# Kernel tuning notes

Measured on AMD Instinct MI355X. Metric: run time of the kernel, lower is better.

Reference implementation:

```python
import jax, jax.numpy as jnp
import numpy as np

N = 250_000          # total event nodes across the batch
E = 1_000_000        # directed edges (radius-graph style, avg degree 4)
B = 25               # graphs in the batch
BS = N // B          # nodes per graph (contiguous blocks)
NX, NY = 8, 9        # ceil(120/16), ceil(100/12) voxel cells for MaxPooling
NC = NX * NY         # 72 voxel cells per graph
M = B * NC           # pooled node slots (empty cells kept but masked)
GRIDS = 16           # MaxPoolingX: 4x4 cells of size (30,25) over 120x100
NOUT = 2
EPS = 1e-5


def spline_basis(p):
    # SplineConv basis: kernel_size=2 per dim, degree=1 open B-spline, dim=3.
    # basis_s(p) = prod_d (p_d if bit_d(s) else 1 - p_d), s = b0 + 2*b1 + 4*b2
    p = jnp.clip(p, 0.0, 1.0)
    cols = []
    for s in range(8):
        w = jnp.ones(p.shape[0], p.dtype)
        for d in range(3):
            w = w * (p[:, d] if (s >> d) & 1 else 1.0 - p[:, d])
        cols.append(w)
    return jnp.stack(cols, axis=1)  # [E, 8]


def spline_conv(x, src, dst, basis, W, emask, num_nodes):
    # SplineConv with aggr='mean', bias=False, root_weight=False
    xj = x[src]                                   # [E, Cin] gather
    msg = jnp.zeros((xj.shape[0], W.shape[2]), x.dtype)
    for s in range(W.shape[0]):                   # 8 kernel weight matrices
        msg = msg + basis[:, s:s + 1] * (xj @ W[s])
    msg = msg * emask[:, None]
    out = jax.ops.segment_sum(msg, dst, num_segments=num_nodes)
    deg = jax.ops.segment_sum(emask, dst, num_segments=num_nodes)
    return out / jnp.maximum(deg, 1.0)[:, None]


def batch_norm(x, gamma, beta, mask=None):
    # BatchNorm1d over nodes (training-mode batch statistics, biased var)
    if mask is None:
        mean = x.mean(axis=0)
        var = jnp.mean((x - mean) ** 2, axis=0)
        return (x - mean) * jax.lax.rsqrt(var + EPS) * gamma + beta
    m = mask.astype(x.dtype)[:, None]
    cnt = jnp.maximum(m.sum(), 1.0)
    mean = (x * m).sum(axis=0) / cnt
    var = (((x - mean) ** 2) * m).sum(axis=0) / cnt
    return ((x - mean) * jax.lax.rsqrt(var + EPS) * gamma + beta) * m


def _forward(x, pos, edge_attr, ws, gs, bs, fc_w, edge_index, batch):
    src, dst = edge_index[0], edge_index[1]
    basis = spline_basis(edge_attr)
    em = jnp.ones((src.shape[0],), x.dtype)
    for i in range(5):  # conv1..conv5 + norm + relu on the full event graph
        x = spline_conv(x, src, dst, basis, ws[i], em, N)
        x = jax.nn.relu(batch_norm(x, gs[i], bs[i]))
    # ---- MaxPooling: voxel grid (16,12) over pos[:, :2], coarsen graph ----
    cx = jnp.clip(jnp.floor(pos[:, 0] / 16.0).astype(jnp.int32), 0, NX - 1)
    cy = jnp.clip(jnp.floor(pos[:, 1] / 12.0).astype(jnp.int32), 0, NY - 1)
    cluster = batch * NC + cy * NX + cx           # [N] -> [0, M)
    cnt = jax.ops.segment_sum(jnp.ones((N,), x.dtype), cluster, num_segments=M)
    nmask = cnt > 0                               # non-empty voxel cells
    xp = jax.ops.segment_max(x, cluster, num_segments=M)
    xp = jnp.where(nmask[:, None], xp, 0.0)       # [M, 32]
    pp = jax.ops.segment_sum(pos, cluster, num_segments=M) / jnp.maximum(cnt, 1.0)[:, None]
    # coarsen edges: remap via cluster, drop self loops, coalesce duplicates
    key = cluster[src] * M + cluster[dst]
    key = jnp.where(cluster[src] == cluster[dst], M * M, key)
    ks = jnp.sort(key)
    dup = jnp.concatenate([jnp.zeros((1,), bool), ks[1:] == ks[:-1]])
    evalid = (ks < M * M) & (~dup)
    rs = jnp.where(evalid, ks // M, 0)
    cs = jnp.where(evalid, ks % M, 0)
    emf = evalid.astype(x.dtype)
    # Cartesian(norm=True, cat=False) on pooled positions
    d = (pp[cs] - pp[rs]) * emf[:, None]
    maxv = jnp.maximum(jnp.max(jnp.abs(d)), 1e-9)
    ea2 = d / (2.0 * maxv) + 0.5
    basis2 = spline_basis(ea2)
    for i in range(5, 7):  # conv6, conv7 on pooled graph
        xp = spline_conv(xp, rs, cs, basis2, ws[i], emf, M)
        xp = jax.nn.relu(batch_norm(xp, gs[i], bs[i], nmask))
    # ---- MaxPoolingX: (30,25) voxel grid -> 4x4 = 16 cells per graph ----
    bcl = jnp.arange(M, dtype=jnp.int32) // NC    # batch id of each cluster
    gx = jnp.clip(jnp.floor(pp[:, 0] / 30.0).astype(jnp.int32), 0, 3)
    gy = jnp.clip(jnp.floor(pp[:, 1] / 25.0).astype(jnp.int32), 0, 3)
    seg = jnp.where(nmask, bcl * GRIDS + gy * 4 + gx, B * GRIDS)
    xg = jax.ops.segment_max(xp, seg, num_segments=B * GRIDS + 1)[:B * GRIDS]
    xg = jnp.where(jnp.isfinite(xg), xg, 0.0)     # empty cells -> 0
    feat = xg.reshape(B, GRIDS * 32)              # [B, 512]
    return feat @ fc_w.T                          # [B, NOUT]


def setup_inputs() -> dict:
    key = jax.random.key(0)
    k = jax.random.split(key, 16)
    x = jax.random.uniform(k[0], (N, 1), dtype=jnp.float32)
    pos = jax.random.uniform(k[1], (N, 3), dtype=jnp.float32) * jnp.array([120.0, 100.0, 1.0], jnp.float32)
    batch = (jnp.arange(N) // BS).astype(jnp.int32)
    src = jax.random.randint(k[2], (E,), 0, N, dtype=jnp.int32)
    dst = (src // BS) * BS + jax.random.randint(k[3], (E,), 0, BS, dtype=jnp.int32)
    edge_index = jnp.stack([src, dst])
    edge_attr = jax.random.uniform(k[4], (E, 3), dtype=jnp.float32)
    chans = [1, 8, 16, 16, 16, 32, 32, 32]
    inp = {"x": x, "pos": pos, "edge_attr": edge_attr}
    for i in range(7):
        cin, cout = chans[i], chans[i + 1]
        inp[f"w{i+1}"] = jax.random.normal(k[5 + i], (8, cin, cout), jnp.float32) / np.sqrt(8.0 * cin)
    for i in range(7):
        inp[f"g{i+1}"] = jnp.ones((chans[i + 1],), jnp.float32)
    for i in range(7):
        inp[f"b{i+1}"] = jnp.zeros((chans[i + 1],), jnp.float32)
    inp["fc_w"] = jax.random.normal(k[12], (NOUT, GRIDS * 32), jnp.float32) * 0.05
    inp["edge_index"] = edge_index
    inp["batch"] = batch
    return inp


def reference(x, pos, edge_attr, w1, w2, w3, w4, w5, w6, w7,
              g1, g2, g3, g4, g5, g6, g7,
              b1, b2, b3, b4, b5, b6, b7, fc_w, edge_index, batch):
    ws = (w1, w2, w3, w4, w5, w6, w7)
    gs = (g1, g2, g3, g4, g5, g6, g7)
    bs = (b1, b2, b3, b4, b5, b6, b7)
    return _forward(x, pos, edge_attr, ws, gs, bs, fc_w, edge_index, batch)
```

## Files before the change

kernel.cpp:

```cpp
#include <hip/hip_runtime.h>

constexpr int NN   = 250000;
constexpr int NE   = 1000000;
constexpr int NBm  = 25;
constexpr int BSg  = NN / NBm;
constexpr int NCc  = 72;
constexpr int MM   = NBm * NCc;
constexpr int PRES = NBm * NCc * NCc;
constexpr int NBK  = NBm * 16;
constexpr float EPSbn = 1e-5f;


__global__ __launch_bounds__(256) void k_deg(const int* __restrict__ dst, int* __restrict__ deg, int n) {
    int e = blockIdx.x * 256 + threadIdx.x;
    if (e < n) atomicAdd(&deg[dst[e]], 1);
}

__global__ __launch_bounds__(256) void k_dhist(const int* __restrict__ deg, const int* __restrict__ batch,
                                               int* __restrict__ dhist, int n) {
    __shared__ int h[NBK];
    int tid = threadIdx.x;
    for (int i = tid; i < NBK; i += 256) h[i] = 0;
    __syncthreads();
    int i = blockIdx.x * 256 + tid;
    if (i < n) atomicAdd(&h[batch[i] * 16 + (15 - min(deg[i], 15))], 1);
    __syncthreads();
    for (int b = tid; b < NBK; b += 256) if (h[b]) atomicAdd(&dhist[b], h[b]);
}

__global__ __launch_bounds__(256) void k_dscan(const int* __restrict__ dhist, int* __restrict__ dcur) {
    __shared__ int tmp[NBK];
    int t = threadIdx.x;
    for (int i = t; i < NBK; i += 256) tmp[i] = dhist[i];
    __syncthreads();
    if (t == 0) { int run = 0; for (int i = 0; i < NBK; i++) { int v = tmp[i]; tmp[i] = run; run += v; } }
    __syncthreads();
    for (int i = t; i < NBK; i += 256) dcur[i] = tmp[i];
}

__global__ __launch_bounds__(256) void k_dscat(const int* __restrict__ deg, const int* __restrict__ batch,
                                               const float* __restrict__ x_in,
                                               int* __restrict__ dcur, int* __restrict__ pinv,
                                               int* __restrict__ deg_p, float* __restrict__ xin_p, int n) {
    __shared__ int lcnt[NBK];
    __shared__ int gbase[NBK];
    int tid = threadIdx.x;
    for (int i = tid; i < NBK; i += 256) lcnt[i] = 0;
    __syncthreads();
    int i = blockIdx.x * 256 + tid;
    int b = 0, rank = 0;
    if (i < n) {
        b = batch[i] * 16 + (15 - min(deg[i], 15));
        rank = atomicAdd(&lcnt[b], 1);
    }
    __syncthreads();
    for (int k = tid; k < NBK; k += 256)
        if (lcnt[k]) gbase[k] = atomicAdd(&dcur[k], lcnt[k]);
    __syncthreads();
    if (i < n) {
        int slot = gbase[b] + rank;
        pinv[i] = slot;
        deg_p[slot] = deg[i];
        xin_p[slot] = x_in[i];
    }
}

__global__ __launch_bounds__(256) void k_scan1(const int* __restrict__ in, int n,
                                               int* __restrict__ outEx, int* __restrict__ bsum) {
    __shared__ int lds[256];
    int t = threadIdx.x;
    int base = blockIdx.x * 2048;
    int v[8]; int s = 0;
#pragma unroll
    for (int i = 0; i < 8; i++) { int idx = base + t * 8 + i; v[i] = (idx < n) ? in[idx] : 0; s += v[i]; }
    lds[t] = s; __syncthreads();
    for (int o = 1; o < 256; o <<= 1) {
        int x = (t >= o) ? lds[t - o] : 0; __syncthreads();
        lds[t] += x; __syncthreads();
    }
    if (t == 255) bsum[blockIdx.x] = lds[255];
    int run = lds[t] - s;
#pragma unroll
    for (int i = 0; i < 8; i++) { int idx = base + t * 8 + i; if (idx < n) outEx[idx] = run; run += v[i]; }
}

__global__ __launch_bounds__(256) void k_scan2(int* bsum, int nb) {
    __shared__ int l[256];
    int t = threadIdx.x;
    int v = (t < nb) ? bsum[t] : 0;
    l[t] = v; __syncthreads();
    for (int o = 1; o < 256; o <<= 1) {
        int x = (t >= o) ? l[t - o] : 0; __syncthreads();
        l[t] += x; __syncthreads();
    }
    if (t < nb) bsum[t] = l[t] - v;
}

__global__ __launch_bounds__(256) void k_scan3(int* __restrict__ outEx, int n, const int* __restrict__ bsum) {
    int i = blockIdx.x * 256 + threadIdx.x;
    if (i < n) outEx[i] += bsum[i >> 11];
}

__global__ __launch_bounds__(256) void k_scatter(const int* __restrict__ src, const int* __restrict__ dst,
                                                 const float* __restrict__ ea, const int* __restrict__ offx,
                                                 const int* __restrict__ pinv,
                                                 int* __restrict__ cursor, float4* __restrict__ erec, int n) {
    int e = blockIdx.x * 256 + threadIdx.x;
    if (e >= n) return;
    int d = pinv[dst[e]];
    int j = offx[d] + atomicAdd(&cursor[d], 1);
    float p0 = fminf(fmaxf(ea[e * 3 + 0], 0.f), 1.f);
    float p1 = fminf(fmaxf(ea[e * 3 + 1], 0.f), 1.f);
    float p2 = fminf(fmaxf(ea[e * 3 + 2], 0.f), 1.f);
    erec[j] = make_float4(__int_as_float(pinv[src[e]]), p0, p1, p2);
}

__global__ __launch_bounds__(256) void k_cluster(const float* __restrict__ pos, const int* __restrict__ pinv,
                                                 int* __restrict__ cluster, int* __restrict__ cluster_p,
                                                 int* __restrict__ cnt, float* __restrict__ ppsum) {
    __shared__ int lcnt[NCc];
    __shared__ float lpp[NCc * 3];
    int tid = threadIdx.x;
    int g = blockIdx.x >> 3, part = blockIdx.x & 7;
    for (int i = tid; i < NCc; i += 256) lcnt[i] = 0;
    for (int i = tid; i < NCc * 3; i += 256) lpp[i] = 0.f;
    __syncthreads();
    int base = g * BSg + part * (BSg / 8);
    int lim = BSg / 8;
    for (int k = tid; k < lim; k += 256) {
        int i = base + k;
        float px = pos[i * 3], py = pos[i * 3 + 1], pz = pos[i * 3 + 2];
        int cx = min(max((int)floorf(px / 16.f), 0), 7);
        int cy = min(max((int)floorf(py / 12.f), 0), 8);
        int lc = cy * 8 + cx;
        cluster[i] = g * NCc + lc;
        cluster_p[pinv[i]] = g * NCc + lc;
        atomicAdd(&lcnt[lc], 1);
        atomicAdd(&lpp[lc * 3 + 0], px);
        atomicAdd(&lpp[lc * 3 + 1], py);
        atomicAdd(&lpp[lc * 3 + 2], pz);
    }
    __syncthreads();
    for (int c = tid; c < NCc; c += 256) {
        if (lcnt[c]) {
            atomicAdd(&cnt[g * NCc + c], lcnt[c]);
            atomicAdd(&ppsum[(g * NCc + c) * 3 + 0], lpp[c * 3 + 0]);
            atomicAdd(&ppsum[(g * NCc + c) * 3 + 1], lpp[c * 3 + 1]);
            atomicAdd(&ppsum[(g * NCc + c) * 3 + 2], lpp[c * 3 + 2]);
        }
    }
}

__global__ __launch_bounds__(256) void k_coarse(const int* __restrict__ src, const int* __restrict__ dst,
                                                const int* __restrict__ cluster, unsigned char* __restrict__ presence,
                                                int n) {
    int e = blockIdx.x * 256 + threadIdx.x;
    if (e >= n) return;
    int r = cluster[src[e]], c = cluster[dst[e]];
    if (r == c) return;
    int g = r / NCc;
    presence[g * (NCc * NCc) + (r % NCc) * NCc + (c % NCc)] = 1;
}

__global__ __launch_bounds__(256) void k_fpp(const int* __restrict__ cnt, const float* __restrict__ ppsum,
                                             float* __restrict__ pp, int* __restrict__ nmask, int* __restrict__ nmc) {
    int m = blockIdx.x * 256 + threadIdx.x;
    if (m >= MM) return;
    int c = cnt[m];
    float inv = 1.f / (float)max(c, 1);
    pp[m * 3 + 0] = ppsum[m * 3 + 0] * inv;
    pp[m * 3 + 1] = ppsum[m * 3 + 1] * inv;
    pp[m * 3 + 2] = ppsum[m * 3 + 2] * inv;
    nmask[m] = (c > 0);
    if (c > 0) atomicAdd(nmc, 1);
}

__global__ __launch_bounds__(256) void k_maxv(const unsigned char* __restrict__ presence, const float* __restrict__ pp,
                                              float* __restrict__ maxv) {
    int i = blockIdx.x * 256 + threadIdx.x;
    float m = 0.f;
    if (i < PRES && presence[i]) {
        int g = i / (NCc * NCc), rem = i % (NCc * NCc);
        int r = g * NCc + rem / NCc, c = g * NCc + rem % NCc;
        float d0 = fabsf(pp[c * 3 + 0] - pp[r * 3 + 0]);
        float d1 = fabsf(pp[c * 3 + 1] - pp[r * 3 + 1]);
        float d2 = fabsf(pp[c * 3 + 2] - pp[r * 3 + 2]);
        m = fmaxf(fmaxf(d0, d1), d2);
    }
    for (int o = 32; o; o >>= 1) m = fmaxf(m, __shfl_xor(m, o));
    if ((threadIdx.x & 63) == 0) atomicMax((int*)maxv, __float_as_int(m));
}


template <int CIN, int COUT, int TPN, bool BN>
__global__ __launch_bounds__(256) void k_conv(
    const float* __restrict__ x, const float4* __restrict__ erec,
    const int* __restrict__ off, const int* __restrict__ deg,
    const float* __restrict__ W, const float* __restrict__ st,
    const float* __restrict__ gam, const float* __restrict__ bet, float invcnt,
    float* __restrict__ out, float* __restrict__ stG, int nwaves) {
    constexpr int CPT = CIN / TPN;
    constexpr int SLICE = COUT + 4;
    constexpr int NPW = 128 / TPN;
    constexpr int CPG = (BSg + NPW - 1) / NPW;
    constexpr int WPG = (CPG + 1) / 2;
    constexpr int NH = (COUT > 16) ? 2 : 1;
    constexpr int OH = COUT / NH;
    constexpr int CWH = OH / TPN;
    __shared__ float Ws[8 * CIN * SLICE];
    __shared__ float ssum[COUT], ssq[COUT];
    int tid = threadIdx.x;
    for (int idx = tid; idx < 8 * CIN * COUT; idx += 256) {
        int s = idx / (CIN * COUT), r = idx % (CIN * COUT);
        int ci = r / COUT, co = r % COUT;
        int t_ = ci / CPT, i_ = ci % CPT;
        Ws[((s * CPT + i_) * TPN + t_) * SLICE + co] = W[idx];
    }
    if (tid < COUT) { ssum[tid] = 0.f; ssq[tid] = 0.f; }
    __syncthreads();

    int w = blockIdx.x * 4 + (tid >> 6);
    int lane = tid & 63;
    int t = lane & (TPN - 1);
    int qi = lane / TPN;
    bool wact = (w < nwaves);
    int g = wact ? (w / WPG) : 0;
    int p = wact ? (w % WPG) : 0;

    float sc[CPT], sh[CPT];
    if constexpr (BN) {
#pragma unroll
        for (int i = 0; i < CPT; i++) {
            int c = t * CPT + i;
            float mean = st[c] * invcnt;
            float var = st[CIN + c] * invcnt - mean * mean;
            float s = rsqrtf(var + EPSbn) * gam[c];
            sc[i] = s; sh[i] = bet[c] - mean * s;
        }
    }

    for (int rep = 0; rep < 2; rep++) {
        if (!wact) break;
        int c = rep ? (CPG - 1 - p) : p;
        if (rep && c == p) break;
        int base = g * BSg + c * NPW;
        int lim = min(NPW, BSg - c * NPW);
        int no = 2 * qi;
        bool act = no < lim;
        int n0 = base + no;

        float agg[2][8 * CPT];
#pragma unroll
        for (int r = 0; r < 2; r++)
#pragma unroll
            for (int i = 0; i < 8 * CPT; i++) agg[r][i] = 0.f;

        int dg0 = 0, dg1 = 0, jb0 = 0, jb1 = 0;
        if (act) {
            jb0 = off[n0];     dg0 = deg[n0];
            jb1 = off[n0 + 1]; dg1 = deg[n0 + 1];
        }
        int mx = max(dg0, dg1);
        int cl0 = max(dg0 - 1, 0), cl1 = max(dg1 - 1, 0);
        float4 rec0 = erec[min(jb0, NE - 1)];
        float4 rec1 = erec[min(jb1, NE - 1)];
        for (int m = 0; m < mx; m++) {
            int s0 = __float_as_int(rec0.x);
            int s1 = __float_as_int(rec1.x);
            const float* xs0 = &x[(size_t)s0 * CIN + t * CPT];
            const float* xs1 = &x[(size_t)s1 * CIN + t * CPT];
            float xv0[CPT], xv1[CPT];
            if constexpr (CPT == 4) {
                float4 v0 = *(const float4*)xs0;
                float4 v1 = *(const float4*)xs1;
                xv0[0] = v0.x; xv0[1] = v0.y; xv0[2] = v0.z; xv0[3] = v0.w;
                xv1[0] = v1.x; xv1[1] = v1.y; xv1[2] = v1.z; xv1[3] = v1.w;
            } else if constexpr (CPT == 8) {
#pragma unroll
                for (int i = 0; i < 8; i += 4) {
                    float4 v0 = *(const float4*)&xs0[i];
                    float4 v1 = *(const float4*)&xs1[i];
                    xv0[i] = v0.x; xv0[i + 1] = v0.y; xv0[i + 2] = v0.z; xv0[i + 3] = v0.w;
                    xv1[i] = v1.x; xv1[i + 1] = v1.y; xv1[i + 2] = v1.z; xv1[i + 3] = v1.w;
                }
            } else {
#pragma unroll
                for (int i = 0; i < CPT; i++) { xv0[i] = xs0[i]; xv1[i] = xs1[i]; }
            }
            float4 nrec0 = erec[jb0 + min(m + 1, cl0)];
            float4 nrec1 = erec[jb1 + min(m + 1, cl1)];
            float f0 = (m < dg0) ? 1.f : 0.f;
            float f1 = (m < dg1) ? 1.f : 0.f;
            if constexpr (BN) {
#pragma unroll
                for (int i = 0; i < CPT; i++) {
                    float a = xv0[i] * sc[i] + sh[i]; xv0[i] = a > 0.f ? a : 0.f;
                    float b = xv1[i] * sc[i] + sh[i]; xv1[i] = b > 0.f ? b : 0.f;
                }
            }
            {
                float p0 = rec0.y, p1 = rec0.z;
                float p2 = rec0.w * f0, q2 = (1.f - rec0.w) * f0;
                float q0 = 1.f - p0, q1 = 1.f - p1;
                float a00 = q0 * q1, a10 = p0 * q1, a01 = q0 * p1, a11 = p0 * p1;
                float bbv[8] = {a00 * q2, a10 * q2, a01 * q2, a11 * q2,
                                a00 * p2, a10 * p2, a01 * p2, a11 * p2};
#pragma unroll
                for (int k = 0; k < 8; k++)
#pragma unroll
                    for (int i = 0; i < CPT; i++) agg[0][k * CPT + i] += bbv[k] * xv0[i];
            }
            {
                float p0 = rec1.y, p1 = rec1.z;
                float p2 = rec1.w * f1, q2 = (1.f - rec1.w) * f1;
                float q0 = 1.f - p0, q1 = 1.f - p1;
                float a00 = q0 * q1, a10 = p0 * q1, a01 = q0 * p1, a11 = p0 * p1;
                float bbv[8] = {a00 * q2, a10 * q2, a01 * q2, a11 * q2,
                                a00 * p2, a10 * p2, a01 * p2, a11 * p2};
#pragma unroll
                for (int k = 0; k < 8; k++)
#pragma unroll
                    for (int i = 0; i < CPT; i++) agg[1][k * CPT + i] += bbv[k] * xv1[i];
            }
            rec0 = nrec0; rec1 = nrec1;
        }

        float inv0 = 1.f / (float)max(dg0, 1);
        float inv1 = 1.f / (float)max(dg1, 1);

#pragma unroll
        for (int h = 0; h < NH; h++) {
            float o0[OH], o1[OH];
#pragma unroll
            for (int c2 = 0; c2 < OH; c2++) { o0[c2] = 0.f; o1[c2] = 0.f; }
#pragma unroll
            for (int k = 0; k < 8; k++)
#pragma unroll
                for (int i = 0; i < CPT; i++) {
                    float a0 = agg[0][k * CPT + i];
                    float a1 = agg[1][k * CPT + i];
                    const float4* wr = (const float4*)&Ws[((k * CPT + i) * TPN + t) * SLICE + h * OH];
#pragma unroll
                    for (int c2 = 0; c2 < OH / 4; c2++) {
                        float4 wv = wr[c2];
                        o0[4 * c2 + 0] += a0 * wv.x; o0[4 * c2 + 1] += a0 * wv.y;
                        o0[4 * c2 + 2] += a0 * wv.z; o0[4 * c2 + 3] += a0 * wv.w;
                        o1[4 * c2 + 0] += a1 * wv.x; o1[4 * c2 + 1] += a1 * wv.y;
                        o1[4 * c2 + 2] += a1 * wv.z; o1[4 * c2 + 3] += a1 * wv.w;
                    }
                }
#pragma unroll
            for (int m = 1; m < TPN; m <<= 1)
#pragma unroll
                for (int c2 = 0; c2 < OH; c2++) { o0[c2] += __shfl_xor(o0[c2], m); o1[c2] += __shfl_xor(o1[c2], m); }

            float v0[CWH], v1[CWH], sv[CWH], qv[CWH];
#pragma unroll
            for (int c2 = 0; c2 < CWH; c2++) {
                v0[c2] = act ? o0[t * CWH + c2] * inv0 : 0.f;
                v1[c2] = act ? o1[t * CWH + c2] * inv1 : 0.f;
                sv[c2] = v0[c2] + v1[c2];
                qv[c2] = v0[c2] * v0[c2] + v1[c2] * v1[c2];
            }
            if (act) {
                float* op0 = &out[(size_t)n0 * COUT + h * OH + t * CWH];
                float* op1 = op0 + COUT;
#pragma unroll
                for (int c2 = 0; c2 < CWH; c2++) { op0[c2] = v0[c2]; op1[c2] = v1[c2]; }
            }
#pragma unroll
            for (int m = TPN; m < 64; m <<= 1)
#pragma unroll
                for (int c2 = 0; c2 < CWH; c2++) { sv[c2] += __shfl_xor(sv[c2], m); qv[c2] += __shfl_xor(qv[c2], m); }
            if (lane < TPN) {
#pragma unroll
                for (int c2 = 0; c2 < CWH; c2++) {
                    atomicAdd(&ssum[h * OH + t * CWH + c2], sv[c2]);
                    atomicAdd(&ssq[h * OH + t * CWH + c2], qv[c2]);
                }
            }
        }
    }
    __syncthreads();
    if (tid < COUT) atomicAdd(&stG[tid], ssum[tid]);
    else if (tid < 2 * COUT) atomicAdd(&stG[tid], ssq[tid - COUT]);
}

template <int C>
__global__ __launch_bounds__(256) void k_stats(const float* __restrict__ x, int rows, float* __restrict__ st) {
    __shared__ float ls[256], lq[256];
    int t = threadIdx.x;
    int gid = blockIdx.x * 256 + t;
    int c = t % C;
    int r0 = gid / C;
    int rstride = (gridDim.x * 256) / C;
    float s = 0.f, q = 0.f;
    for (int r = r0; r < rows; r += rstride) { float v = x[(size_t)r * C + c]; s += v; q += v * v; }
    ls[t] = s; lq[t] = q;
    __syncthreads();
    if (t < C) {
        float ss = 0.f, qq = 0.f;
        for (int k = t; k < 256; k += C) { ss += ls[k]; qq += lq[k]; }
        atomicAdd(&st[c], ss); atomicAdd(&st[C + c], qq);
    }
}

__global__ __launch_bounds__(256) void k_pool(const float* __restrict__ x, const int* __restrict__ cluster_p,
                                              const float* __restrict__ st, const float* __restrict__ gam,
                                              const float* __restrict__ bet, float invcnt,
                                              float* __restrict__ xp) {
    __shared__ float cellv[NCc * 32];
    __shared__ float scs[32], shs[32];
    int tid = threadIdx.x;
    int g = blockIdx.x >> 3, part = blockIdx.x & 7;
    for (int i = tid; i < NCc * 32; i += 256) cellv[i] = 0.f;
    if (tid < 32) {
        float mean = st[tid] * invcnt;
        float var = st[32 + tid] * invcnt - mean * mean;
        float s = rsqrtf(var + EPSbn) * gam[tid];
        scs[tid] = s; shs[tid] = bet[tid] - mean * s;
    }
    __syncthreads();
    int base = g * BSg + part * (BSg / 8);
    const int nelem = (BSg / 8) * 32;
    for (int ii = tid; ii < nelem; ii += 256) {
        int nd = base + (ii >> 5), ch = ii & 31;
        float v = x[(size_t)nd * 32 + ch] * scs[ch] + shs[ch];
        v = v > 0.f ? v : 0.f;
        int lc = cluster_p[nd] - g * NCc;
        atomicMax((int*)&cellv[lc * 32 + ch], __float_as_int(v));
    }
    __syncthreads();
    for (int ii = tid; ii < NCc * 32; ii += 256)
        atomicMax((int*)&xp[g * NCc * 32 + ii], __float_as_int(cellv[ii]));
}

__global__ __launch_bounds__(256) void k_y(const float* __restrict__ xp, const float* __restrict__ W,
                                           float* __restrict__ y) {
    int i = blockIdx.x * 256 + threadIdx.x;
    if (i >= MM * 256) return;
    int r = i >> 8, rem = i & 255, s = rem >> 5, co = rem & 31;
    const float* xr = &xp[r * 32];
    const float* w = &W[s * 1024 + co];
    float a = 0.f;
#pragma unroll
    for (int ci = 0; ci < 32; ci++) a += xr[ci] * w[ci * 32];
    y[i] = a;
}

__global__ __launch_bounds__(256) void k_convp(const float* __restrict__ y, const float* __restrict__ pp,
                                               const unsigned char* __restrict__ presence,
                                               const float* __restrict__ maxv, float* __restrict__ out) {
    int i = blockIdx.x * 256 + threadIdx.x;
    if (i >= MM * 32) return;
    int c = i >> 5, co = i & 31;
    int g = c / NCc, lc = c % NCc;
    float mv = fmaxf(maxv[0], 1e-9f);
    float inv2 = 0.5f / mv;
    float pcx = pp[c * 3], pcy = pp[c * 3 + 1], pcz = pp[c * 3 + 2];
    const unsigned char* pr = &presence[g * (NCc * NCc) + lc];
    float acc = 0.f; int dg = 0;
    for (int lr = 0; lr < NCc; lr++) {
        if (pr[lr * NCc]) {
            dg++;
            int r = g * NCc + lr;
            float p0 = fminf(fmaxf((pcx - pp[r * 3]) * inv2 + 0.5f, 0.f), 1.f);
            float p1 = fminf(fmaxf((pcy - pp[r * 3 + 1]) * inv2 + 0.5f, 0.f), 1.f);
            float p2 = fminf(fmaxf((pcz - pp[r * 3 + 2]) * inv2 + 0.5f, 0.f), 1.f);
            float q0 = 1.f - p0, q1 = 1.f - p1, q2 = 1.f - p2;
            const float* yr = &y[r * 256 + co];
            acc += (q0 * q1 * q2) * yr[0]   + (p0 * q1 * q2) * yr[32]
                 + (q0 * p1 * q2) * yr[64]  + (p0 * p1 * q2) * yr[96]
                 + (q0 * q1 * p2) * yr[128] + (p0 * q1 * p2) * yr[160]
                 + (q0 * p1 * p2) * yr[192] + (p0 * p1 * p2) * yr[224];
        }
    }
    out[i] = acc / (float)max(dg, 1);
}

__global__ __launch_bounds__(256) void k_bnp(float* __restrict__ xp, const float* __restrict__ st,
                                             const float* __restrict__ gam, const float* __restrict__ bet,
                                             const int* __restrict__ nmask, const int* __restrict__ nmc) {
    int i = blockIdx.x * 256 + threadIdx.x;
    if (i >= MM * 32) return;
    int m = i >> 5, ch = i & 31;
    float cnt = (float)max(nmc[0], 1);
    float mean = st[ch] / cnt;
    float var = st[32 + ch] / cnt - mean * mean;
    float s = rsqrtf(var + EPSbn) * gam[ch];
    float v = xp[i] * s + (bet[ch] - mean * s);
    v = v > 0.f ? v : 0.f;
    xp[i] = nmask[m] ? v : 0.f;
}

__global__ __launch_bounds__(256) void k_poolX(const float* __restrict__ xp, const float* __restrict__ pp,
                                               const int* __restrict__ nmask, float* __restrict__ xg) {
    int i = blockIdx.x * 256 + threadIdx.x;
    if (i >= MM * 32) return;
    int m = i >> 5, ch = i & 31;
    if (!nmask[m]) return;
    int g = m / NCc;
    int gx = min(max((int)floorf(pp[m * 3] / 30.f), 0), 3);
    int gy = min(max((int)floorf(pp[m * 3 + 1] / 25.f), 0), 3);
    int seg = g * 16 + gy * 4 + gx;
    atomicMax((int*)&xg[seg * 32 + ch], __float_as_int(xp[i]));
}

__global__ __launch_bounds__(64) void k_fc(const float* __restrict__ xg, const float* __restrict__ fcw,
                                           float* __restrict__ out) {
    int q = blockIdx.x;
    int b = q >> 1, o = q & 1;
    int l = threadIdx.x;
    float a = 0.f;
    for (int k = l; k < 512; k += 64) a += xg[b * 512 + k] * fcw[o * 512 + k];
    for (int s = 32; s; s >>= 1) a += __shfl_xor(a, s);
    if (l == 0) out[b * 2 + o] = a;
}


extern "C" void kernel_launch(void* const* d_in, const int* in_sizes, int n_in,
                              void* d_out, int out_size, void* d_ws, size_t ws_size,
                              hipStream_t stream) {
    const float* x_in  = (const float*)d_in[0];
    const float* pos   = (const float*)d_in[1];
    const float* eattr = (const float*)d_in[2];
    const float* w[7];  for (int i = 0; i < 7; i++) w[i]  = (const float*)d_in[3 + i];
    const float* gm[7]; for (int i = 0; i < 7; i++) gm[i] = (const float*)d_in[10 + i];
    const float* bt[7]; for (int i = 0; i < 7; i++) bt[i] = (const float*)d_in[17 + i];
    const float* fcw   = (const float*)d_in[24];
    const int* ei      = (const int*)d_in[25];
    const int* batch   = (const int*)d_in[26];
    const int* esrc = ei;
    const int* edst = ei + NE;
    float* outp = (float*)d_out;

    char* base = (char*)d_ws;
    size_t cur = 0;
    auto alloc = [&](size_t elems) -> void* {
        void* p = base + cur;
        cur += (((elems * 4) + 255) & ~(size_t)255);
        return p;
    };
    int*   deg_i     = (int*)alloc(NN);
    int*   cursor    = (int*)alloc(NN);
    int*   cnt_i     = (int*)alloc(MM);
    float* ppsum     = (float*)alloc(MM * 3);
    unsigned char* presence = (unsigned char*)alloc(PRES / 4);
    float* maxv      = (float*)alloc(64);
    int*   nmc       = (int*)alloc(64);
    int*   dhist     = (int*)alloc(NBK);
    float* st        = (float*)alloc(7 * 64);
    float* xp_pool   = (float*)alloc(MM * 32);
    float* xg        = (float*)alloc(NBm * 16 * 32);
    size_t zero_bytes = cur;
    int*   off_ex    = (int*)alloc(NN);
    int*   bsum      = (int*)alloc(256);
    int*   cluster   = (int*)alloc(NN);
    int*   cluster_p = (int*)alloc(NN);
    int*   dcur      = (int*)alloc(NBK);
    int*   pinv      = (int*)alloc(NN);
    int*   deg_p     = (int*)alloc(NN);
    float* xin_p     = (float*)alloc(NN);
    float4* erec     = (float4*)alloc((size_t)NE * 4);
    float* x_a       = (float*)alloc((size_t)NN * 32);
    float* x_b       = (float*)alloc((size_t)NN * 16);
    float* pp        = (float*)alloc(MM * 3);
    int*   nmask     = (int*)alloc(MM);
    float* ybuf      = (float*)alloc(MM * 256);
    float* pt0       = (float*)alloc(MM * 32);
    float* pt1       = (float*)alloc(MM * 32);
    (void)ws_size; (void)in_sizes; (void)n_in; (void)out_size;

    (void)hipMemsetAsync(d_ws, 0, zero_bytes, stream);

    int gE = (NE + 255) / 256;
    int gN = (NN + 255) / 256;
    int nbS = (NN + 2047) / 2048;

    k_deg<<<gE, 256, 0, stream>>>(edst, deg_i, NE);
    k_dhist<<<gN, 256, 0, stream>>>(deg_i, batch, dhist, NN);
    k_dscan<<<1, 256, 0, stream>>>(dhist, dcur);
    k_dscat<<<gN, 256, 0, stream>>>(deg_i, batch, x_in, dcur, pinv, deg_p, xin_p, NN);
    k_scan1<<<nbS, 256, 0, stream>>>(deg_p, NN, off_ex, bsum);
    k_scan2<<<1, 256, 0, stream>>>(bsum, nbS);
    k_scan3<<<gN, 256, 0, stream>>>(off_ex, NN, bsum);
    k_scatter<<<gE, 256, 0, stream>>>(esrc, edst, eattr, off_ex, pinv, cursor, erec, NE);
    k_cluster<<<NBm * 8, 256, 0, stream>>>(pos, pinv, cluster, cluster_p, cnt_i, ppsum);
    k_coarse<<<gE, 256, 0, stream>>>(esrc, edst, cluster, presence, NE);
    k_fpp<<<(MM + 255) / 256, 256, 0, stream>>>(cnt_i, ppsum, pp, nmask, nmc);
    k_maxv<<<(PRES + 255) / 256, 256, 0, stream>>>(presence, pp, maxv);

    const float invN = 1.f / (float)NN;
    constexpr int W1 = NBm * ((((BSg + 127) / 128) + 1) / 2);
    constexpr int W2 = NBm * ((((BSg + 63) / 64) + 1) / 2);
    constexpr int W4 = NBm * ((((BSg + 31) / 32) + 1) / 2);
    k_conv<1, 8, 1, false><<<(W1 + 3) / 4, 256, 0, stream>>>(xin_p, erec, off_ex, deg_p,
                                                             w[0], nullptr, nullptr, nullptr, 0.f, x_a, st + 0, W1);
    k_conv<8, 16, 2, true><<<(W2 + 3) / 4, 256, 0, stream>>>(x_a, erec, off_ex, deg_p,
                                                             w[1], st + 0, gm[0], bt[0], invN, x_b, st + 64, W2);
    k_conv<16, 16, 4, true><<<(W4 + 3) / 4, 256, 0, stream>>>(x_b, erec, off_ex, deg_p,
                                                              w[2], st + 64, gm[1], bt[1], invN, x_a, st + 128, W4);
    k_conv<16, 16, 4, true><<<(W4 + 3) / 4, 256, 0, stream>>>(x_a, erec, off_ex, deg_p,
                                                              w[3], st + 128, gm[2], bt[2], invN, x_b, st + 192, W4);
    k_conv<16, 32, 4, true><<<(W4 + 3) / 4, 256, 0, stream>>>(x_b, erec, off_ex, deg_p,
                                                              w[4], st + 192, gm[3], bt[3], invN, x_a, st + 256, W4);
    k_pool<<<NBm * 8, 256, 0, stream>>>(x_a, cluster_p, st + 256, gm[4], bt[4], invN, xp_pool);
    k_y<<<(MM * 256 + 255) / 256, 256, 0, stream>>>(xp_pool, w[5], ybuf);
    k_convp<<<(MM * 32 + 255) / 256, 256, 0, stream>>>(ybuf, pp, presence, maxv, pt0);
    k_stats<32><<<8, 256, 0, stream>>>(pt0, MM, st + 320);
    k_bnp<<<(MM * 32 + 255) / 256, 256, 0, stream>>>(pt0, st + 320, gm[5], bt[5], nmask, nmc);
    k_y<<<(MM * 256 + 255) / 256, 256, 0, stream>>>(pt0, w[6], ybuf);
    k_convp<<<(MM * 32 + 255) / 256, 256, 0, stream>>>(ybuf, pp, presence, maxv, pt1);
    k_stats<32><<<8, 256, 0, stream>>>(pt1, MM, st + 384);
    k_bnp<<<(MM * 32 + 255) / 256, 256, 0, stream>>>(pt1, st + 384, gm[6], bt[6], nmask, nmc);
    k_poolX<<<(MM * 32 + 255) / 256, 256, 0, stream>>>(pt1, pp, nmask, xg);
    k_fc<<<50, 64, 0, stream>>>(xg, fcw, outp);
}
```

Before: 646.7 us.

## Prefetch next neighbor features in conv loop and fuse pooled-layer BN stages

The edge-aggregation loop in k_conv now software-pipelines the neighbor feature gather, loading the next edge's x row while the current one is accumulated. In the pooled stage, the batch-norm statistics are folded into k_convp, BN+ReLU is applied on the fly in a new k_y2 and in k_poolX, and k_stats and k_bnp are removed. The aim is to hide gather latency and cut several small kernel launches. The prefetch costs extra registers, and the stats are still reduced through shared and global atomics.

```diff
diff --git a/kernel.cpp b/kernel.cpp
--- a/kernel.cpp
+++ b/kernel.cpp
@@ -264,33 +264,56 @@
         int cl0 = max(dg0 - 1, 0), cl1 = max(dg1 - 1, 0);
         float4 rec0 = erec[min(jb0, NE - 1)];
         float4 rec1 = erec[min(jb1, NE - 1)];
-        for (int m = 0; m < mx; m++) {
-            int s0 = __float_as_int(rec0.x);
-            int s1 = __float_as_int(rec1.x);
-            const float* xs0 = &x[(size_t)s0 * CIN + t * CPT];
-            const float* xs1 = &x[(size_t)s1 * CIN + t * CPT];
-            float xv0[CPT], xv1[CPT];
+        float4 nrec0 = erec[jb0 + min(1, cl0)];
+        float4 nrec1 = erec[jb1 + min(1, cl1)];
+        float xc0[CPT], xc1[CPT];
+        {
+            const float* xs0 = &x[(size_t)__float_as_int(rec0.x) * CIN + t * CPT];
+            const float* xs1 = &x[(size_t)__float_as_int(rec1.x) * CIN + t * CPT];
             if constexpr (CPT == 4) {
-                float4 v0 = *(const float4*)xs0;
-                float4 v1 = *(const float4*)xs1;
-                xv0[0] = v0.x; xv0[1] = v0.y; xv0[2] = v0.z; xv0[3] = v0.w;
-                xv1[0] = v1.x; xv1[1] = v1.y; xv1[2] = v1.z; xv1[3] = v1.w;
+                float4 v0 = *(const float4*)xs0; float4 v1 = *(const float4*)xs1;
+                xc0[0] = v0.x; xc0[1] = v0.y; xc0[2] = v0.z; xc0[3] = v0.w;
+                xc1[0] = v1.x; xc1[1] = v1.y; xc1[2] = v1.z; xc1[3] = v1.w;
             } else if constexpr (CPT == 8) {
 #pragma unroll
                 for (int i = 0; i < 8; i += 4) {
-                    float4 v0 = *(const float4*)&xs0[i];
-                    float4 v1 = *(const float4*)&xs1[i];
-                    xv0[i] = v0.x; xv0[i + 1] = v0.y; xv0[i + 2] = v0.z; xv0[i + 3] = v0.w;
-                    xv1[i] = v1.x; xv1[i + 1] = v1.y; xv1[i + 2] = v1.z; xv1[i + 3] = v1.w;
+                    float4 v0 = *(const float4*)&xs0[i]; float4 v1 = *(const float4*)&xs1[i];
+                    xc0[i] = v0.x; xc0[i + 1] = v0.y; xc0[i + 2] = v0.z; xc0[i + 3] = v0.w;
+                    xc1[i] = v1.x; xc1[i + 1] = v1.y; xc1[i + 2] = v1.z; xc1[i + 3] = v1.w;
                 }
             } else {
 #pragma unroll
-                for (int i = 0; i < CPT; i++) { xv0[i] = xs0[i]; xv1[i] = xs1[i]; }
-            }
-            float4 nrec0 = erec[jb0 + min(m + 1, cl0)];
-            float4 nrec1 = erec[jb1 + min(m + 1, cl1)];
+                for (int i = 0; i < CPT; i++) { xc0[i] = xs0[i]; xc1[i] = xs1[i]; }
+            }
+        }
+        for (int m = 0; m < mx; m++) {
+            float xn0[CPT], xn1[CPT];
+            {
+                const float* xs0 = &x[(size_t)__float_as_int(nrec0.x) * CIN + t * CPT];
+                const float* xs1 = &x[(size_t)__float_as_int(nrec1.x) * CIN + t * CPT];
+                if constexpr (CPT == 4) {
+                    float4 v0 = *(const float4*)xs0; float4 v1 = *(const float4*)xs1;
+                    xn0[0] = v0.x; xn0[1] = v0.y; xn0[2] = v0.z; xn0[3] = v0.w;
+                    xn1[0] = v1.x; xn1[1] = v1.y; xn1[2] = v1.z; xn1[3] = v1.w;
+                } else if constexpr (CPT == 8) {
+#pragma unroll
+                    for (int i = 0; i < 8; i += 4) {
+                        float4 v0 = *(const float4*)&xs0[i]; float4 v1 = *(const float4*)&xs1[i];
+                        xn0[i] = v0.x; xn0[i + 1] = v0.y; xn0[i + 2] = v0.z; xn0[i + 3] = v0.w;
+                        xn1[i] = v1.x; xn1[i + 1] = v1.y; xn1[i + 2] = v1.z; xn1[i + 3] = v1.w;
+                    }
+                } else {
+#pragma unroll
+                    for (int i = 0; i < CPT; i++) { xn0[i] = xs0[i]; xn1[i] = xs1[i]; }
+                }
+            }
+            float4 nn0 = erec[jb0 + min(m + 2, cl0)];
+            float4 nn1 = erec[jb1 + min(m + 2, cl1)];
             float f0 = (m < dg0) ? 1.f : 0.f;
             float f1 = (m < dg1) ? 1.f : 0.f;
+            float xv0[CPT], xv1[CPT];
+#pragma unroll
+            for (int i = 0; i < CPT; i++) { xv0[i] = xc0[i]; xv1[i] = xc1[i]; }
             if constexpr (BN) {
 #pragma unroll
                 for (int i = 0; i < CPT; i++) {
@@ -323,6 +346,9 @@
                     for (int i = 0; i < CPT; i++) agg[1][k * CPT + i] += bbv[k] * xv1[i];
             }
             rec0 = nrec0; rec1 = nrec1;
+            nrec0 = nn0; nrec1 = nn1;
+#pragma unroll
+            for (int i = 0; i < CPT; i++) { xc0[i] = xn0[i]; xc1[i] = xn1[i]; }
         }
 
         float inv0 = 1.f / (float)max(dg0, 1);
@@ -384,25 +410,6 @@
     __syncthreads();
     if (tid < COUT) atomicAdd(&stG[tid], ssum[tid]);
     else if (tid < 2 * COUT) atomicAdd(&stG[tid], ssq[tid - COUT]);
-}
-
-template <int C>
-__global__ __launch_bounds__(256) void k_stats(const float* __restrict__ x, int rows, float* __restrict__ st) {
-    __shared__ float ls[256], lq[256];
-    int t = threadIdx.x;
-    int gid = blockIdx.x * 256 + t;
-    int c = t % C;
-    int r0 = gid / C;
-    int rstride = (gridDim.x * 256) / C;
-    float s = 0.f, q = 0.f;
-    for (int r = r0; r < rows; r += rstride) { float v = x[(size_t)r * C + c]; s += v; q += v * v; }
-    ls[t] = s; lq[t] = q;
-    __syncthreads();
-    if (t < C) {
-        float ss = 0.f, qq = 0.f;
-        for (int k = t; k < 256; k += C) { ss += ls[k]; qq += lq[k]; }
-        atomicAdd(&st[c], ss); atomicAdd(&st[C + c], qq);
-    }
 }
 
 __global__ __launch_bounds__(256) void k_pool(const float* __restrict__ x, const int* __restrict__ cluster_p,
@@ -448,11 +455,46 @@
     y[i] = a;
 }
 
+__global__ __launch_bounds__(256) void k_y2(const float* __restrict__ pt, const float* __restrict__ W,
+                                            const float* __restrict__ st, const float* __restrict__ gam,
+                                            const float* __restrict__ bet, const int* __restrict__ nmask,
+                                            const int* __restrict__ nmc, float* __restrict__ y) {
+    __shared__ float scs[32], shs[32];
+    int tid = threadIdx.x;
+    if (tid < 32) {
+        float cntf = (float)max(nmc[0], 1);
+        float mean = st[tid] / cntf;
+        float var = st[32 + tid] / cntf - mean * mean;
+        float s = rsqrtf(var + EPSbn) * gam[tid];
+        scs[tid] = s; shs[tid] = bet[tid] - mean * s;
+    }
+    __syncthreads();
+    int i = blockIdx.x * 256 + tid;
+    if (i >= MM * 256) return;
+    int r = i >> 8, rem = i & 255, s = rem >> 5, co = rem & 31;
+    float a = 0.f;
+    if (nmask[r]) {
+        const float* xr = &pt[r * 32];
+        const float* w = &W[s * 1024 + co];
+#pragma unroll
+        for (int ci = 0; ci < 32; ci++) {
+            float v = xr[ci] * scs[ci] + shs[ci];
+            v = v > 0.f ? v : 0.f;
+            a += v * w[ci * 32];
+        }
+    }
+    y[i] = a;
+}
+
 __global__ __launch_bounds__(256) void k_convp(const float* __restrict__ y, const float* __restrict__ pp,
                                                const unsigned char* __restrict__ presence,
-                                               const float* __restrict__ maxv, float* __restrict__ out) {
-    int i = blockIdx.x * 256 + threadIdx.x;
-    if (i >= MM * 32) return;
+                                               const float* __restrict__ maxv, float* __restrict__ out,
+                                               float* __restrict__ stG) {
+    __shared__ float ssum[32], ssq[32];
+    int tid = threadIdx.x;
+    if (tid < 32) { ssum[tid] = 0.f; ssq[tid] = 0.f; }
+    __syncthreads();
+    int i = blockIdx.x * 256 + tid;
     int c = i >> 5, co = i & 31;
     int g = c / NCc, lc = c % NCc;
     float mv = fmaxf(maxv[0], 1e-9f);
@@ -475,35 +517,36 @@
                  + (q0 * p1 * p2) * yr[192] + (p0 * p1 * p2) * yr[224];
         }
     }
-    out[i] = acc / (float)max(dg, 1);
-}
-
-__global__ __launch_bounds__(256) void k_bnp(float* __restrict__ xp, const float* __restrict__ st,
-                                             const float* __restrict__ gam, const float* __restrict__ bet,
-                                             const int* __restrict__ nmask, const int* __restrict__ nmc) {
-    int i = blockIdx.x * 256 + threadIdx.x;
-    if (i >= MM * 32) return;
-    int m = i >> 5, ch = i & 31;
-    float cnt = (float)max(nmc[0], 1);
-    float mean = st[ch] / cnt;
-    float var = st[32 + ch] / cnt - mean * mean;
-    float s = rsqrtf(var + EPSbn) * gam[ch];
-    float v = xp[i] * s + (bet[ch] - mean * s);
-    v = v > 0.f ? v : 0.f;
-    xp[i] = nmask[m] ? v : 0.f;
-}
-
-__global__ __launch_bounds__(256) void k_poolX(const float* __restrict__ xp, const float* __restrict__ pp,
-                                               const int* __restrict__ nmask, float* __restrict__ xg) {
+    float val = acc / (float)max(dg, 1);
+    out[i] = val;
+    float sv = val, qv = val * val;
+    sv += __shfl_xor(sv, 32); qv += __shfl_xor(qv, 32);
+    int lane = tid & 63;
+    if (lane < 32) { atomicAdd(&ssum[lane], sv); atomicAdd(&ssq[lane], qv); }
+    __syncthreads();
+    if (tid < 32) atomicAdd(&stG[tid], ssum[tid]);
+    else if (tid < 64) atomicAdd(&stG[32 + tid - 32], ssq[tid - 32]);
+}
+
+__global__ __launch_bounds__(256) void k_poolX(const float* __restrict__ pt, const float* __restrict__ pp,
+                                               const float* __restrict__ st, const float* __restrict__ gam,
+                                               const float* __restrict__ bet, const int* __restrict__ nmask,
+                                               const int* __restrict__ nmc, float* __restrict__ xg) {
     int i = blockIdx.x * 256 + threadIdx.x;
     if (i >= MM * 32) return;
     int m = i >> 5, ch = i & 31;
     if (!nmask[m]) return;
+    float cntf = (float)max(nmc[0], 1);
+    float mean = st[ch] / cntf;
+    float var = st[32 + ch] / cntf - mean * mean;
+    float s = rsqrtf(var + EPSbn) * gam[ch];
+    float v = pt[i] * s + (bet[ch] - mean * s);
+    v = v > 0.f ? v : 0.f;
     int g = m / NCc;
     int gx = min(max((int)floorf(pp[m * 3] / 30.f), 0), 3);
     int gy = min(max((int)floorf(pp[m * 3 + 1] / 25.f), 0), 3);
     int seg = g * 16 + gy * 4 + gx;
-    atomicMax((int*)&xg[seg * 32 + ch], __float_as_int(xp[i]));
+    atomicMax((int*)&xg[seg * 32 + ch], __float_as_int(v));
 }
 
 __global__ __launch_bounds__(64) void k_fc(const float* __restrict__ xg, const float* __restrict__ fcw,
@@ -606,13 +649,9 @@
                                                               w[4], st + 192, gm[3], bt[3], invN, x_a, st + 256, W4);
     k_pool<<<NBm * 8, 256, 0, stream>>>(x_a, cluster_p, st + 256, gm[4], bt[4], invN, xp_pool);
     k_y<<<(MM * 256 + 255) / 256, 256, 0, stream>>>(xp_pool, w[5], ybuf);
-    k_convp<<<(MM * 32 + 255) / 256, 256, 0, stream>>>(ybuf, pp, presence, maxv, pt0);
-    k_stats<32><<<8, 256, 0, stream>>>(pt0, MM, st + 320);
-    k_bnp<<<(MM * 32 + 255) / 256, 256, 0, stream>>>(pt0, st + 320, gm[5], bt[5], nmask, nmc);
-    k_y<<<(MM * 256 + 255) / 256, 256, 0, stream>>>(pt0, w[6], ybuf);
-    k_convp<<<(MM * 32 + 255) / 256, 256, 0, stream>>>(ybuf, pp, presence, maxv, pt1);
-    k_stats<32><<<8, 256, 0, stream>>>(pt1, MM, st + 384);
-    k_bnp<<<(MM * 32 + 255) / 256, 256, 0, stream>>>(pt1, st + 384, gm[6], bt[6], nmask, nmc);
-    k_poolX<<<(MM * 32 + 255) / 256, 256, 0, stream>>>(pt1, pp, nmask, xg);
+    k_convp<<<(MM * 32) / 256, 256, 0, stream>>>(ybuf, pp, presence, maxv, pt0, st + 320);
+    k_y2<<<(MM * 256 + 255) / 256, 256, 0, stream>>>(pt0, w[6], st + 320, gm[5], bt[5], nmask, nmc, ybuf);
+    k_convp<<<(MM * 32) / 256, 256, 0, stream>>>(ybuf, pp, presence, maxv, pt1, st + 384);
+    k_poolX<<<(MM * 32 + 255) / 256, 256, 0, stream>>>(pt1, pp, st + 384, gm[6], bt[6], nmask, nmc, xg);
     k_fc<<<50, 64, 0, stream>>>(xg, fcw, outp);
 }
```

Result: faster. 630.0 us (-2.6%).
